# Kernel optimization log

Hardware: AMD Instinct MI355X
Metric: run time of the kernel (lower is better)

The kernel has to match this reference:

```python
import jax, jax.numpy as jnp
import numpy as np

B, N, DIM, HID = 128, 4096, 16, 128

def _linear_init(key, fan_in, fan_out):
    # torch nn.Linear default: U(-1/sqrt(fan_in), 1/sqrt(fan_in))
    kw, kb = jax.random.split(key)
    bound = 1.0 / np.sqrt(fan_in)
    W = jax.random.uniform(kw, (fan_in, fan_out), minval=-bound, maxval=bound, dtype=jnp.float32)
    b = jax.random.uniform(kb, (fan_out,), minval=-bound, maxval=bound, dtype=jnp.float32)
    return W, b

def setup_inputs() -> dict:
    key = jax.random.key(0)
    ks = jax.random.split(key, 8)
    x = jax.random.normal(ks[0], (B, N, DIM), dtype=jnp.float32)
    adj_col = (jax.random.uniform(ks[1], (N,), dtype=jnp.float32) > 0.5).astype(jnp.float32)
    W_n2e, b_n2e = _linear_init(ks[2], 2 * DIM, HID)
    W_e2e, b_e2e = _linear_init(ks[3], HID, HID)
    W_e2n, b_e2n = _linear_init(ks[4], HID, HID)
    W_n2n, b_n2n = _linear_init(ks[5], HID, HID)
    W_out, b_out = _linear_init(ks[6], DIM + HID, DIM)
    return {"x": x, "adj_col": adj_col,
            "W_n2e": W_n2e, "b_n2e": b_n2e,
            "W_e2e": W_e2e, "b_e2e": b_e2e,
            "W_e2n": W_e2n, "b_e2n": b_e2n,
            "W_n2n": W_n2n, "b_n2n": b_n2n,
            "W_out": W_out, "b_out": b_out,
            "i": 0}

def reference(x, adj_col, W_n2e, b_n2e, W_e2e, b_e2e, W_e2n, b_e2n, W_n2n, b_n2n, W_out, b_out, i):
    starter = x                                        # [B, N, dim]
    ender = x[:, i, :][:, None, :]                     # [B, 1, dim]
    ender = jnp.broadcast_to(ender, starter.shape)     # [B, N, dim]
    h = jnp.concatenate([starter, ender], axis=2)      # [B, N, 2*dim]
    h = jax.nn.relu(h @ W_n2e + b_n2e)                 # [B, N, hid]
    h = jax.nn.relu(h @ W_e2e + b_e2e)                 # [B, N, hid]
    h = h * adj_col[None, :, None]                     # adjacency mask
    h = jnp.sum(h, axis=1)                             # [B, hid]
    h = jax.nn.relu(h @ W_e2n + b_e2n)
    h = jax.nn.relu(h @ W_n2n + b_n2n)
    h = jnp.concatenate([starter[:, i, :], h], axis=-1)  # [B, dim+hid]
    return h @ W_out + b_out                           # [B, dim]
```

## Files before the change

### kernel.cpp

```cpp
#include <hip/hip_runtime.h>
#include <hip/hip_bf16.h>

#define B_    128
#define N_    4096
#define DIM_  16
#define HID_  128
#define NT_   4
#define ROWS_ (N_ / NT_)

typedef __bf16 bf16x8 __attribute__((ext_vector_type(8)));
typedef float floatx16 __attribute__((ext_vector_type(16)));
typedef unsigned int u32;

__device__ inline bf16x8 load_cvt8(const float* __restrict__ p) {
  const float4 u = *(const float4*)p;
  const float4 v = *(const float4*)(p + 4);
  bf16x8 r;
  r[0] = (__bf16)u.x; r[1] = (__bf16)u.y; r[2] = (__bf16)u.z; r[3] = (__bf16)u.w;
  r[4] = (__bf16)v.x; r[5] = (__bf16)v.y; r[6] = (__bf16)v.z; r[7] = (__bf16)v.w;
  return r;
}

__global__ __launch_bounds__(256, 2) void edge_kernel(
    const float* __restrict__ x, const float* __restrict__ adj,
    const float* __restrict__ W1, const float* __restrict__ b1,
    const float* __restrict__ W2, const float* __restrict__ b2,
    const int* __restrict__ ip, float* __restrict__ part)
{
  __shared__ __align__(16) __bf16 sW2[HID_ * HID_];
  __shared__ __align__(16) float sW1s[DIM_][HID_];
  __shared__ int   sIdx[ROWS_ + 192];
  __shared__ float sAcc[HID_];
  __shared__ float sB1[HID_];
  __shared__ float sEnder[DIM_];
  __shared__ int   sCnt;

  const int t  = threadIdx.x;
  const int b  = blockIdx.y;
  const int n0 = blockIdx.x * ROWS_;
  const int ii = __ldg(ip);

  const int wave = t >> 6, lane = t & 63;
  const int half = lane >> 5, l31 = lane & 31;
  const int rg = wave >> 1;
  const int ch = wave & 1;

  if (t == 0) sCnt = 0;
  if (t < HID_) sAcc[t] = 0.f;
  if (t < DIM_) sEnder[t] = x[((size_t)b * N_ + ii) * DIM_ + t];
  __syncthreads();

  #pragma unroll
  for (int r = t; r < ROWS_; r += 256) {
    const bool act = adj[n0 + r] != 0.f;
    const unsigned long long m = __ballot(act);
    int base = 0;
    if (lane == 0) base = atomicAdd(&sCnt, __popcll(m));
    base = __shfl(base, 0);
    if (act) {
      const int pre = __builtin_amdgcn_mbcnt_hi((u32)(m >> 32),
                      __builtin_amdgcn_mbcnt_lo((u32)m, 0));
      sIdx[base + pre] = n0 + r;
    }
  }

  #pragma unroll
  for (int e = t; e < DIM_ * HID_; e += 256) sW1s[e >> 7][e & 127] = W1[e];

  #pragma unroll
  for (int e = 0; e < 8; ++e) {
    const int G = t * 8 + e;
    const int c = G >> 4, gg = G & 15;
    bf16x8 v;
    #pragma unroll
    for (int j = 0; j < 8; ++j) {
      const int row = ((gg >> 1) << 4) + ((j >> 2) << 3) + ((gg & 1) << 2) + (j & 3);
      v[j] = (__bf16)W2[row * HID_ + c];
    }
    *(bf16x8*)&sW2[(c << 7) + ((gg ^ (c & 15)) << 3)] = v;
  }

  if (t < HID_) {
    float s = b1[t];
    #pragma unroll
    for (int k = 0; k < DIM_; ++k) s += sEnder[k] * W1[(DIM_ + k) * HID_ + t];
    sB1[t] = s;
  }

  const float bv0 = b2[ch * 64 + l31], bv1 = b2[ch * 64 + 32 + l31];

  __syncthreads();
  const int cnt = sCnt;
  const int nch64 = (cnt + 63) >> 6;
  const int end = nch64 * 64;
  for (int p = cnt + t; p < end + 128; p += 256) sIdx[p] = n0;

  bf16x8 w1f[4];
  #pragma unroll
  for (int ft = 0; ft < 4; ++ft) {
    bf16x8 v;
    #pragma unroll
    for (int j = 0; j < 8; ++j) v[j] = (__bf16)sW1s[half * 8 + j][ft * 32 + l31];
    w1f[ft] = v;
  }

  bf16x8 w2r[16];
  {
    const int c0 = ch * 64 + l31;
    const __bf16* base0 = &sW2[(c0 << 7)];
    const __bf16* base1 = &sW2[((c0 + 32) << 7)];
    #pragma unroll
    for (int s = 0; s < 8; ++s) {
      const int gp = ((s << 1) + half) ^ (c0 & 15);
      w2r[s]     = *(const bf16x8*)(base0 + (gp << 3));
      w2r[8 + s] = *(const bf16x8*)(base1 + (gp << 3));
    }
  }

  bf16x8 a2f[4], onef;
  #pragma unroll
  for (int j = 0; j < 8; ++j) onef[j] = (__bf16)0.f;
  if (half == 0) { onef[0] = (__bf16)1.f; onef[1] = (__bf16)1.f; }
  #pragma unroll
  for (int ft = 0; ft < 4; ++ft) {
    bf16x8 v;
    #pragma unroll
    for (int j = 0; j < 8; ++j) v[j] = (__bf16)0.f;
    if (half == 0) {
      const float s = sB1[ft * 32 + l31];
      const __bf16 hi = (__bf16)s;
      v[0] = hi;
      v[1] = (__bf16)(s - (float)hi);
    }
    a2f[ft] = v;
  }
  __syncthreads();

  float sum0 = 0.f, sum1 = 0.f;
  floatx16 zf;
  #pragma unroll
  for (int r = 0; r < 16; ++r) zf[r] = 0.f;

  int cb = rg * 32;
  bf16x8 xf;
  {
    const int row = sIdx[cb + l31];
    xf = load_cvt8(&x[((size_t)b * N_ + row) * DIM_ + half * 8]);
  }

  for (; cb < end; cb += 64) {
    const int nrow = sIdx[cb + 64 + l31];

    bf16x8 af[8];
    #pragma unroll
    for (int ft = 0; ft < 4; ++ft) {
      floatx16 hc = __builtin_amdgcn_mfma_f32_32x32x16_bf16(w1f[ft], xf, zf, 0, 0, 0);
      hc = __builtin_amdgcn_mfma_f32_32x32x16_bf16(a2f[ft], onef, hc, 0, 0, 0);
      bf16x8 a0, a1;
      #pragma unroll
      for (int j = 0; j < 8; ++j) {
        a0[j] = (__bf16)fmaxf(hc[j],     0.f);
        a1[j] = (__bf16)fmaxf(hc[8 + j], 0.f);
      }
      af[2 * ft]     = a0;
      af[2 * ft + 1] = a1;
    }

    const bf16x8 nxf = load_cvt8(&x[((size_t)b * N_ + nrow) * DIM_ + half * 8]);

    floatx16 c0 = zf, c1 = zf;
    #pragma unroll
    for (int s = 0; s < 8; ++s) {
      c0 = __builtin_amdgcn_mfma_f32_32x32x16_bf16(af[s], w2r[s],     c0, 0, 0, 0);
      c1 = __builtin_amdgcn_mfma_f32_32x32x16_bf16(af[s], w2r[8 + s], c1, 0, 0, 0);
    }

    if (cb + 32 <= cnt) {
      #pragma unroll
      for (int r = 0; r < 16; ++r) {
        sum0 += fmaxf(c0[r] + bv0, 0.f);
        sum1 += fmaxf(c1[r] + bv1, 0.f);
      }
    } else {
      #pragma unroll
      for (int r = 0; r < 16; ++r) {
        const int q = cb + (r & 3) + ((r >> 2) << 3) + (half << 2);
        if (q < cnt) {
          sum0 += fmaxf(c0[r] + bv0, 0.f);
          sum1 += fmaxf(c1[r] + bv1, 0.f);
        }
      }
    }
    xf = nxf;
  }

  sum0 += __shfl_xor(sum0, 32);
  sum1 += __shfl_xor(sum1, 32);
  if (half == 0) {
    atomicAdd(&sAcc[ch * 64 + l31],      sum0);
    atomicAdd(&sAcc[ch * 64 + 32 + l31], sum1);
  }
  __syncthreads();
  if (t < HID_) part[((size_t)b * NT_ + blockIdx.x) * HID_ + t] = sAcc[t];
}

__global__ void tail_kernel(
    const float* __restrict__ x, const float* __restrict__ part,
    const float* __restrict__ W3, const float* __restrict__ b3,
    const float* __restrict__ W4, const float* __restrict__ b4,
    const float* __restrict__ W5, const float* __restrict__ b5,
    const int* __restrict__ ip, float* __restrict__ out)
{
  const int b = blockIdx.x, t = threadIdx.x;
  __shared__ float s0[HID_], s1[HID_], s2[HID_], se[DIM_];
  const int ii = __ldg(ip);
  if (t < DIM_) se[t] = x[((size_t)b * N_ + ii) * DIM_ + t];
  float a = 0.f;
  #pragma unroll
  for (int p = 0; p < NT_; ++p) a += part[((size_t)b * NT_ + p) * HID_ + t];
  s0[t] = a;
  __syncthreads();
  float v = b3[t];
  #pragma unroll 16
  for (int k = 0; k < HID_; ++k) v += s0[k] * W3[k * HID_ + t];
  s1[t] = fmaxf(v, 0.f);
  __syncthreads();
  float w = b4[t];
  #pragma unroll 16
  for (int k = 0; k < HID_; ++k) w += s1[k] * W4[k * HID_ + t];
  s2[t] = fmaxf(w, 0.f);
  __syncthreads();
  if (t < DIM_) {
    float o = b5[t];
    #pragma unroll
    for (int k = 0; k < DIM_; ++k) o += se[k] * W5[k * DIM_ + t];
    #pragma unroll 16
    for (int k = 0; k < HID_; ++k) o += s2[k] * W5[(DIM_ + k) * DIM_ + t];
    out[b * DIM_ + t] = o;
  }
}

extern "C" void kernel_launch(void* const* d_in, const int* in_sizes, int n_in,
                              void* d_out, int out_size, void* d_ws, size_t ws_size,
                              hipStream_t stream) {
  const float* x   = (const float*)d_in[0];
  const float* adj = (const float*)d_in[1];
  const float* W1  = (const float*)d_in[2];
  const float* b1  = (const float*)d_in[3];
  const float* W2  = (const float*)d_in[4];
  const float* b2  = (const float*)d_in[5];
  const float* W3  = (const float*)d_in[6];
  const float* b3  = (const float*)d_in[7];
  const float* W4  = (const float*)d_in[8];
  const float* b4  = (const float*)d_in[9];
  const float* W5  = (const float*)d_in[10];
  const float* b5  = (const float*)d_in[11];
  const int*   ip  = (const int*)d_in[12];
  float* out  = (float*)d_out;
  float* part = (float*)d_ws;

  edge_kernel<<<dim3(NT_, B_), 256, 0, stream>>>(x, adj, W1, b1, W2, b2, ip, part);
  tail_kernel<<<B_, HID_, 0, stream>>>(x, part, W3, b3, W4, b4, W5, b5, ip, out);
}
```

Baseline: 122.7 us.

## Deepen gather prefetch, coalesce W2 staging, hoist bias, parallelize tail kernel

Prefetches gathered x rows two iterations ahead instead of one to better hide global load latency in the main MFMA loop. W2 staging now uses coalesced float4 loads with scattered bf16 LDS stores instead of strided scalar loads. The bias add inside the ReLU-sum is replaced by max against the negated bias plus a single post-loop correction. The tail kernel uses 256 threads with split-K reductions. The deeper prefetch costs extra registers and may pressure occupancy.

```diff
diff --git a/kernel.cpp b/kernel.cpp
--- a/kernel.cpp
+++ b/kernel.cpp
@@ -68,16 +68,20 @@
   for (int e = t; e < DIM_ * HID_; e += 256) sW1s[e >> 7][e & 127] = W1[e];
 
   #pragma unroll
-  for (int e = 0; e < 8; ++e) {
-    const int G = t * 8 + e;
-    const int c = G >> 4, gg = G & 15;
-    bf16x8 v;
-    #pragma unroll
-    for (int j = 0; j < 8; ++j) {
-      const int row = ((gg >> 1) << 4) + ((j >> 2) << 3) + ((gg & 1) << 2) + (j & 3);
-      v[j] = (__bf16)W2[row * HID_ + c];
-    }
-    *(bf16x8*)&sW2[(c << 7) + ((gg ^ (c & 15)) << 3)] = v;
+  for (int i = 0; i < 16; ++i) {
+    const int i2 = (i + (t >> 2)) & 15;
+    const int Lbase = (i2 * 256 + t) * 4;
+    const float4 v4 = *(const float4*)&W2[Lbase];
+    const int row = Lbase >> 7;
+    const int gg  = ((row >> 4) << 1) | ((row >> 2) & 1);
+    const int j   = (((row >> 3) & 1) << 2) | (row & 3);
+    const int cb0 = Lbase & 127;
+    #pragma unroll
+    for (int w = 0; w < 4; ++w) {
+      const float fv = (w == 0) ? v4.x : (w == 1) ? v4.y : (w == 2) ? v4.z : v4.w;
+      const int c = cb0 + w;
+      sW2[(c << 7) + ((gg ^ (c & 15)) << 3) + j] = (__bf16)fv;
+    }
   }
 
   if (t < HID_) {
@@ -88,6 +92,7 @@
   }
 
   const float bv0 = b2[ch * 64 + l31], bv1 = b2[ch * 64 + 32 + l31];
+  const float nb0 = -bv0, nb1 = -bv1;
 
   __syncthreads();
   const int cnt = sCnt;
@@ -137,24 +142,27 @@
   __syncthreads();
 
   float sum0 = 0.f, sum1 = 0.f;
+  int nfull = 0;
   floatx16 zf;
   #pragma unroll
   for (int r = 0; r < 16; ++r) zf[r] = 0.f;
 
   int cb = rg * 32;
-  bf16x8 xf;
+  bf16x8 xf0, xf1;
   {
-    const int row = sIdx[cb + l31];
-    xf = load_cvt8(&x[((size_t)b * N_ + row) * DIM_ + half * 8]);
+    const int r0 = sIdx[cb + l31];
+    xf0 = load_cvt8(&x[((size_t)b * N_ + r0) * DIM_ + half * 8]);
+    const int r1 = sIdx[cb + 64 + l31];
+    xf1 = load_cvt8(&x[((size_t)b * N_ + r1) * DIM_ + half * 8]);
   }
 
   for (; cb < end; cb += 64) {
-    const int nrow = sIdx[cb + 64 + l31];
+    const int nrow = sIdx[cb + 128 + l31];
 
     bf16x8 af[8];
     #pragma unroll
     for (int ft = 0; ft < 4; ++ft) {
-      floatx16 hc = __builtin_amdgcn_mfma_f32_32x32x16_bf16(w1f[ft], xf, zf, 0, 0, 0);
+      floatx16 hc = __builtin_amdgcn_mfma_f32_32x32x16_bf16(w1f[ft], xf0, zf, 0, 0, 0);
       hc = __builtin_amdgcn_mfma_f32_32x32x16_bf16(a2f[ft], onef, hc, 0, 0, 0);
       bf16x8 a0, a1;
       #pragma unroll
@@ -166,7 +174,7 @@
       af[2 * ft + 1] = a1;
     }
 
-    const bf16x8 nxf = load_cvt8(&x[((size_t)b * N_ + nrow) * DIM_ + half * 8]);
+    const bf16x8 xf2 = load_cvt8(&x[((size_t)b * N_ + nrow) * DIM_ + half * 8]);
 
     floatx16 c0 = zf, c1 = zf;
     #pragma unroll
@@ -176,10 +184,11 @@
     }
 
     if (cb + 32 <= cnt) {
+      ++nfull;
       #pragma unroll
       for (int r = 0; r < 16; ++r) {
-        sum0 += fmaxf(c0[r] + bv0, 0.f);
-        sum1 += fmaxf(c1[r] + bv1, 0.f);
+        sum0 += fmaxf(c0[r], nb0);
+        sum1 += fmaxf(c1[r], nb1);
       }
     } else {
       #pragma unroll
@@ -191,8 +200,11 @@
         }
       }
     }
-    xf = nxf;
-  }
+    xf0 = xf1; xf1 = xf2;
+  }
+  const float fn = (float)nfull * 16.f;
+  sum0 = fmaf(fn, bv0, sum0);
+  sum1 = fmaf(fn, bv1, sum1);
 
   sum0 += __shfl_xor(sum0, 32);
   sum1 += __shfl_xor(sum1, 32);
@@ -204,7 +216,7 @@
   if (t < HID_) part[((size_t)b * NT_ + blockIdx.x) * HID_ + t] = sAcc[t];
 }
 
-__global__ void tail_kernel(
+__global__ __launch_bounds__(256) void tail_kernel(
     const float* __restrict__ x, const float* __restrict__ part,
     const float* __restrict__ W3, const float* __restrict__ b3,
     const float* __restrict__ W4, const float* __restrict__ b4,
@@ -212,31 +224,56 @@
     const int* __restrict__ ip, float* __restrict__ out)
 {
   const int b = blockIdx.x, t = threadIdx.x;
+  const int col = t & 127, kh = t >> 7;
   __shared__ float s0[HID_], s1[HID_], s2[HID_], se[DIM_];
+  __shared__ float sp[2][HID_];
+  __shared__ float so[16][DIM_];
   const int ii = __ldg(ip);
   if (t < DIM_) se[t] = x[((size_t)b * N_ + ii) * DIM_ + t];
-  float a = 0.f;
-  #pragma unroll
-  for (int p = 0; p < NT_; ++p) a += part[((size_t)b * NT_ + p) * HID_ + t];
-  s0[t] = a;
-  __syncthreads();
-  float v = b3[t];
-  #pragma unroll 16
-  for (int k = 0; k < HID_; ++k) v += s0[k] * W3[k * HID_ + t];
-  s1[t] = fmaxf(v, 0.f);
-  __syncthreads();
-  float w = b4[t];
-  #pragma unroll 16
-  for (int k = 0; k < HID_; ++k) w += s1[k] * W4[k * HID_ + t];
-  s2[t] = fmaxf(w, 0.f);
+  if (t < HID_) {
+    float a = 0.f;
+    #pragma unroll
+    for (int p = 0; p < NT_; ++p) a += part[((size_t)b * NT_ + p) * HID_ + t];
+    s0[t] = a;
+  }
+  __syncthreads();
+  float v = 0.f;
+  #pragma unroll 32
+  for (int q = 0; q < 64; ++q) {
+    const int k = kh * 64 + q;
+    v += s0[k] * W3[k * HID_ + col];
+  }
+  sp[kh][col] = v;
+  __syncthreads();
+  if (t < HID_) s1[t] = fmaxf(b3[t] + sp[0][t] + sp[1][t], 0.f);
+  __syncthreads();
+  float w = 0.f;
+  #pragma unroll 32
+  for (int q = 0; q < 64; ++q) {
+    const int k = kh * 64 + q;
+    w += s1[k] * W4[k * HID_ + col];
+  }
+  sp[kh][col] = w;
+  __syncthreads();
+  if (t < HID_) s2[t] = fmaxf(b4[t] + sp[0][t] + sp[1][t], 0.f);
+  __syncthreads();
+  {
+    const int oc = t & 15, seg = t >> 4;
+    float o = 0.f;
+    #pragma unroll
+    for (int q = 0; q < 9; ++q) {
+      const int kk = seg * 9 + q;
+      const float cv = (kk < DIM_) ? se[kk] : s2[kk - DIM_];
+      o += cv * W5[kk * DIM_ + oc];
+    }
+    so[seg][oc] = o;
+  }
   __syncthreads();
   if (t < DIM_) {
-    float o = b5[t];
-    #pragma unroll
-    for (int k = 0; k < DIM_; ++k) o += se[k] * W5[k * DIM_ + t];
-    #pragma unroll 16
-    for (int k = 0; k < HID_; ++k) o += s2[k] * W5[(DIM_ + k) * DIM_ + t];
-    out[b * DIM_ + t] = o;
+    float acc = b5[t];
+    #pragma unroll
+    for (int s = 0; s < 16; ++s) acc += so[s][t];
+    out[b * DIM_ + t] = acc;
   }
 }
 
@@ -260,5 +297,5 @@
   float* part = (float*)d_ws;
 
   edge_kernel<<<dim3(NT_, B_), 256, 0, stream>>>(x, adj, W1, b1, W2, b2, ip, part);
-  tail_kernel<<<B_, HID_, 0, stream>>>(x, part, W3, b3, W4, b4, W5, b5, ip, out);
+  tail_kernel<<<B_, 256, 0, stream>>>(x, part, W3, b3, W4, b4, W5, b5, ip, out);
 }
```

After: 131.2 us. +6.9%, slower.
